# Optimization experiments

Measured on AMD Instinct MI355X. Metric: run time of the kernel, lower is better.

## Reference

```python
import jax, jax.numpy as jnp
import numpy as np

# 8 corner offsets of the trilinear cell: (8, 3)
_OFFS = jnp.array([[i, j, k] for i in (0, 1) for j in (0, 1) for k in (0, 1)], dtype=jnp.int32)


def _gridding(cloud, R):
    """Trilinear scatter of points into an RxRxR occupancy-weight grid.

    cloud: (b, n, 3) with coords in [-0.5, 0.5] (already divided by scale).
    Returns (b, R, R, R) grid where each point adds trilinear weights to its
    8 neighboring cells (the GRNet gridding_distance forward kernel).
    """
    b, n, _ = cloud.shape
    v = (cloud + 0.5) * R                      # continuous voxel coords in [0, R)
    lower = jnp.floor(v)
    frac = v - lower                           # (b, n, 3) in [0, 1)
    lower = lower.astype(jnp.int32)
    nb = lower[:, :, None, :] + _OFFS[None, None]              # (b, n, 8, 3)
    # per-axis trilinear weight: (1 - frac) for the low corner, frac for the high
    w_d = jnp.where(_OFFS[None, None] == 0,
                    1.0 - frac[:, :, None, :], frac[:, :, None, :])  # (b, n, 8, 3)
    w = jnp.prod(w_d, axis=-1)                                  # (b, n, 8)
    valid = jnp.all((nb >= 0) & (nb < R), axis=-1)              # (b, n, 8)
    w = jnp.where(valid, w, 0.0)
    nbc = jnp.clip(nb, 0, R - 1)
    flat = (nbc[..., 0] * R + nbc[..., 1]) * R + nbc[..., 2]    # (b, n, 8)
    batch_off = jnp.arange(b, dtype=jnp.int32)[:, None, None] * (R * R * R)
    idx = (flat + batch_off).reshape(-1)
    grid = jnp.zeros((b * R * R * R,), cloud.dtype).at[idx].add(w.reshape(-1))
    return grid.reshape(b, R, R, R)


def setup_inputs() -> dict:
    key = jax.random.key(0)
    k1, k2 = jax.random.split(key)
    R = 128
    B, N1, N2 = 16, 65536, 65536
    # coords in [-(R-2)/2, (R-2)/2] so that after /scale they are inside (-0.5, 0.5)
    pred = (jax.random.uniform(k1, (B, N1, 3), jnp.float32) - 0.5) * (R - 2)
    gt = (jax.random.uniform(k2, (B, N2, 3), jnp.float32) - 0.5) * (R - 2)
    return {"pred_cloud": pred, "gt_cloud": gt, "scale": R}


def reference(pred_cloud, gt_cloud, scale):
    pred = pred_cloud / scale
    gt = gt_cloud / scale
    return _gridding(pred, scale), _gridding(gt, scale)
```

## Files before the change

### kernel.cpp

```cpp
#include <hip/hip_runtime.h>
#include <stdint.h>


constexpr int R    = 128;
constexpr int R3c  = R * R * R;
constexpr int BPG  = 256;
constexpr int NBLK = 512;
constexpr int BLKT = 512;
constexpr int NCH  = 8;
constexpr int MAXBINS = 8192;

constexpr size_t WS_HIST = 0;
constexpr size_t WS_CS   = 16u << 20;
constexpr size_t WS_TOT  = 17u << 20;
constexpr size_t WS_BASE = 18u << 20;
constexpr size_t WS_QREC = 20u << 20;
constexpr size_t WS_REC  = 40u << 20;

typedef float f4v __attribute__((ext_vector_type(4)));

__device__ __forceinline__ uint32_t quant1(float p) {
    const float S = 16384.0f;
    const uint32_t QMAX = (126u << 14) | 16383u;
    float v = p + 64.0f;
    return min(__float2uint_rn(fmaxf(v, 0.0f) * S), QMAX);
}

__device__ __forceinline__ uint2 pack_rec(uint32_t xq, uint32_t yq, uint32_t zq) {
    return make_uint2(xq | (yq << 21), (yq >> 11) | (zq << 10));
}
__device__ __forceinline__ void unpack_rec(uint2 r, uint32_t& xq, uint32_t& yq, uint32_t& zq) {
    xq = r.x & 0x1FFFFFu;
    yq = (r.x >> 21) | ((r.y & 0x3FFu) << 11);
    zq = (r.y >> 10) & 0x1FFFFFu;
}

__device__ __forceinline__ void load_point(
    const float* __restrict__ pred, const float* __restrict__ gt,
    int i, int total1, int n1, int n2, int B,
    float& px, float& py, float& pz, int& cb)
{
    const float* p;
    if (i < total1) { p = pred + (size_t)i * 3; cb = i / n1; }
    else { int j = i - total1; p = gt + (size_t)j * 3; cb = B + j / n2; }
    px = p[0]; py = p[1]; pz = p[2];
}

__device__ __forceinline__ void region_range(uint32_t xq, uint32_t yq, uint32_t zq,
                                             int& rx0, int& rx1, int& ry0, int& ry1,
                                             int& rz0, int& rz1)
{
    int ix = xq >> 14, iy = yq >> 14, iz = zq >> 14;
    rx0 = ix >> 4; rx1 = (ix + 1) >> 4;
    ry0 = iy >> 4; ry1 = (iy + 1) >> 4;
    rz0 = iz >> 5; rz1 = (iz + 1) >> 5;
}

__global__ __launch_bounds__(BLKT, 2) void bin_hist_qrec(
    const float* __restrict__ pred, const float* __restrict__ gt,
    int total1, int P, int n1, int n2, int B, int ppb, int vec4ok,
    uint16_t* __restrict__ hist, uint2* __restrict__ qrec, int NBINS)
{
    __shared__ uint32_t h[MAXBINS];
    for (int j = threadIdx.x; j < NBINS; j += BLKT) h[j] = 0;
    __syncthreads();

    int s = blockIdx.x * ppb, e = min(s + ppb, P);
    if (vec4ok) {
        bool isgt = (s >= total1);
        const float* src = isgt ? gt + (size_t)(s - total1) * 3
                                : pred + (size_t)s * 3;
        const int n = isgt ? n2 : n1;
        const int cb0 = isgt ? B : 0;
        const int loff = isgt ? total1 : 0;
        const float4* src4 = (const float4*)src;
        int ngrp = (e - s) >> 2;
        for (int g = threadIdx.x; g < ngrp; g += BLKT) {
            float4 a = src4[g * 3 + 0];
            float4 b4 = src4[g * 3 + 1];
            float4 c4 = src4[g * 3 + 2];
            int li = (s + g * 4) - loff;
            int hbase = (cb0 + li / n) * BPG;
            float xs[4] = {a.x, a.w, b4.z, c4.y};
            float ys[4] = {a.y, b4.x, b4.w, c4.z};
            float zs[4] = {a.z, b4.y, c4.x, c4.w};
            uint2 rec[4];
            #pragma unroll
            for (int q = 0; q < 4; ++q) {
                uint32_t xq = quant1(xs[q]), yq = quant1(ys[q]), zq = quant1(zs[q]);
                rec[q] = pack_rec(xq, yq, zq);
                int rx0, rx1, ry0, ry1, rz0, rz1;
                region_range(xq, yq, zq, rx0, rx1, ry0, ry1, rz0, rz1);
                for (int aa = rx0; aa <= rx1; ++aa)
                    for (int bb = ry0; bb <= ry1; ++bb)
                        for (int cc = rz0; cc <= rz1; ++cc)
                            atomicAdd(&h[hbase + (aa << 5) + (bb << 2) + cc], 1u);
            }
            uint4* q4 = (uint4*)(qrec + (size_t)s + (size_t)g * 4);
            q4[0] = make_uint4(rec[0].x, rec[0].y, rec[1].x, rec[1].y);
            q4[1] = make_uint4(rec[2].x, rec[2].y, rec[3].x, rec[3].y);
        }
    } else {
        for (int i = s + threadIdx.x; i < e; i += BLKT) {
            float px, py, pz; int cb;
            load_point(pred, gt, i, total1, n1, n2, B, px, py, pz, cb);
            uint32_t xq = quant1(px), yq = quant1(py), zq = quant1(pz);
            qrec[i] = pack_rec(xq, yq, zq);
            int rx0, rx1, ry0, ry1, rz0, rz1;
            region_range(xq, yq, zq, rx0, rx1, ry0, ry1, rz0, rz1);
            int base = cb * BPG;
            for (int a = rx0; a <= rx1; ++a)
                for (int b = ry0; b <= ry1; ++b)
                    for (int c = rz0; c <= rz1; ++c)
                        atomicAdd(&h[base + (a << 5) + (b << 2) + c], 1u);
        }
    }
    __syncthreads();
    uint16_t* o = hist + (size_t)blockIdx.x * NBINS;
    for (int j = threadIdx.x; j < NBINS; j += BLKT) o[j] = (uint16_t)h[j];
}

__global__ __launch_bounds__(256) void scan_chunk(
    const uint16_t* __restrict__ hist, uint32_t* __restrict__ cs, int NBINS)
{
    int tid = blockIdx.x * 256 + threadIdx.x;
    if (tid >= NCH * NBINS) return;
    int c = tid / NBINS, j = tid - c * NBINS;
    int b0 = c * (NBLK / NCH);
    uint32_t s = 0;
    for (int b = b0; b < b0 + NBLK / NCH; ++b)
        s += hist[(size_t)b * NBINS + j];
    cs[c * NBINS + j] = s;
}

__global__ __launch_bounds__(256) void scan_fin(
    uint16_t* __restrict__ hist, const uint32_t* __restrict__ cs,
    uint32_t* __restrict__ tot, int NBINS)
{
    int tid = blockIdx.x * 256 + threadIdx.x;
    if (tid >= NCH * NBINS) return;
    int c = tid / NBINS, j = tid - c * NBINS;
    uint32_t run = 0;
    for (int cc = 0; cc < c; ++cc) run += cs[cc * NBINS + j];
    int b0 = c * (NBLK / NCH);
    for (int b = b0; b < b0 + NBLK / NCH; ++b) {
        size_t k = (size_t)b * NBINS + j;
        uint32_t t = hist[k];
        hist[k] = (uint16_t)run;
        run += t;
    }
    if (c == NCH - 1) tot[j] = run;
}

__global__ __launch_bounds__(256) void scan_base(
    const uint32_t* __restrict__ tot, uint32_t* __restrict__ base, int NBINS)
{
    __shared__ uint32_t part[256];
    int t = threadIdx.x;
    int chunk = NBINS / 256;
    uint32_t s = 0;
    for (int i = 0; i < chunk; ++i) s += tot[t * chunk + i];
    part[t] = s;
    __syncthreads();
    if (t == 0) {
        uint32_t run = 0;
        for (int i = 0; i < 256; ++i) { uint32_t v = part[i]; part[i] = run; run += v; }
    }
    __syncthreads();
    uint32_t run = part[t];
    for (int i = 0; i < chunk; ++i) {
        base[t * chunk + i] = run;
        run += tot[t * chunk + i];
    }
    if (t == 255) base[NBINS] = run;
}

__global__ __launch_bounds__(BLKT, 2) void bin_scatter_qrec(
    const uint2* __restrict__ qrec,
    int total1, int P, int n1, int n2, int B, int ppb, int vec4ok,
    const uint16_t* __restrict__ hist, const uint32_t* __restrict__ base,
    uint2* __restrict__ records, int NBINS)
{
    __shared__ uint32_t cur[MAXBINS];
    const uint16_t* hrow = hist + (size_t)blockIdx.x * NBINS;
    for (int j = threadIdx.x; j < NBINS; j += BLKT)
        cur[j] = base[j] + (uint32_t)hrow[j];
    __syncthreads();

    int s = blockIdx.x * ppb, e = min(s + ppb, P);
    if (vec4ok) {
        bool isgt = (s >= total1);
        const int n = isgt ? n2 : n1;
        const int cb0 = isgt ? B : 0;
        const int loff = isgt ? total1 : 0;
        const uint4* qr4 = (const uint4*)(qrec + (size_t)s);
        int ngrp = (e - s) >> 2;
        for (int g = threadIdx.x; g < ngrp; g += BLKT) {
            uint4 q0 = qr4[2 * g];
            uint4 q1 = qr4[2 * g + 1];
            uint2 rec[4] = {make_uint2(q0.x, q0.y), make_uint2(q0.z, q0.w),
                            make_uint2(q1.x, q1.y), make_uint2(q1.z, q1.w)};
            int li = (s + g * 4) - loff;
            int bb = (cb0 + li / n) * BPG;
            #pragma unroll
            for (int q = 0; q < 4; ++q) {
                uint32_t xq, yq, zq;
                unpack_rec(rec[q], xq, yq, zq);
                int rx0, rx1, ry0, ry1, rz0, rz1;
                region_range(xq, yq, zq, rx0, rx1, ry0, ry1, rz0, rz1);
                for (int aa = rx0; aa <= rx1; ++aa)
                    for (int b2 = ry0; b2 <= ry1; ++b2)
                        for (int cc = rz0; cc <= rz1; ++cc) {
                            uint32_t slot =
                                atomicAdd(&cur[bb + (aa << 5) + (b2 << 2) + cc], 1u);
                            records[slot] = rec[q];
                        }
            }
        }
    } else {
        for (int i = s + threadIdx.x; i < e; i += BLKT) {
            int cb;
            if (i < total1) cb = i / n1;
            else            cb = B + (i - total1) / n2;
            uint2 rec = qrec[i];
            uint32_t xq, yq, zq;
            unpack_rec(rec, xq, yq, zq);
            int rx0, rx1, ry0, ry1, rz0, rz1;
            region_range(xq, yq, zq, rx0, rx1, ry0, ry1, rz0, rz1);
            int bb = cb * BPG;
            for (int a = rx0; a <= rx1; ++a)
                for (int b = ry0; b <= ry1; ++b)
                    for (int c = rz0; c <= rz1; ++c) {
                        uint32_t slot = atomicAdd(&cur[bb + (a << 5) + (b << 2) + c], 1u);
                        records[slot] = rec;
                    }
        }
    }
}

__global__ __launch_bounds__(256) void accum_kernel(
    const uint32_t* __restrict__ base, const uint2* __restrict__ records,
    float* __restrict__ out)
{
    __shared__ float tile[16 * 16 * 32];
    int bin = blockIdx.x;
    int cb = bin >> 8;
    int region = bin & 255;
    int rx = region >> 5, ry = (region >> 2) & 7, rz = region & 3;

    float4* t4 = (float4*)tile;
    for (int t = threadIdx.x; t < 2048; t += 256)
        t4[t] = make_float4(0.f, 0.f, 0.f, 0.f);
    __syncthreads();

    uint32_t s = base[bin], e = base[bin + 1];
    const float FQ = 6.103515625e-05f;
    for (uint32_t r = s + threadIdx.x; r < e; r += 256) {
        uint32_t xq, yq, zq;
        unpack_rec(records[r], xq, yq, zq);
        int ix = xq >> 14, iy = yq >> 14, iz = zq >> 14;
        float fx = (float)(xq & 16383u) * FQ;
        float fy = (float)(yq & 16383u) * FQ;
        float fz = (float)(zq & 16383u) * FQ;
        float wx[2] = {1.0f - fx, fx};
        float wy[2] = {1.0f - fy, fy};
        float wz[2] = {1.0f - fz, fz};
        #pragma unroll
        for (int dx = 0; dx < 2; ++dx) {
            int cx = ix + dx;
            if ((cx >> 4) != rx) continue;
            #pragma unroll
            for (int dy = 0; dy < 2; ++dy) {
                int cy = iy + dy;
                if ((cy >> 4) != ry) continue;
                float wxy = wx[dx] * wy[dy];
                #pragma unroll
                for (int dz = 0; dz < 2; ++dz) {
                    int cz = iz + dz;
                    if ((cz >> 5) != rz) continue;
                    atomicAdd(&tile[(((cx & 15) << 4) + (cy & 15)) * 32 + (cz & 31)],
                              wxy * wz[dz]);
                }
            }
        }
    }
    __syncthreads();

    float* gout = out + (size_t)cb * R3c;
    for (int w = threadIdx.x; w < 2048; w += 256) {
        int lin = w * 4;
        int lx = lin >> 9, rem = lin & 511, ly = rem >> 5, lz = rem & 31;
        int X = rx * 16 + lx, Y = ry * 16 + ly, Z = rz * 32 + lz;
        f4v v = ((const f4v*)tile)[w];
        __builtin_nontemporal_store(v, (f4v*)&gout[((size_t)X * R + Y) * R + Z]);
    }
}

__device__ __forceinline__ void point_math_f(float px, float py, float pz,
                                             int& ix, int& iy, int& iz,
                                             float& fx, float& fy, float& fz)
{
    const float inv = 1.0f / 128.0f;
    float vx = (px * inv + 0.5f) * 128.0f;
    float vy = (py * inv + 0.5f) * 128.0f;
    float vz = (pz * inv + 0.5f) * 128.0f;
    float lx = floorf(vx), ly = floorf(vy), lz = floorf(vz);
    fx = vx - lx; fy = vy - ly; fz = vz - lz;
    ix = min(max((int)lx, 0), R - 2);
    iy = min(max((int)ly, 0), R - 2);
    iz = min(max((int)lz, 0), R - 2);
}

__global__ __launch_bounds__(256) void gridding_scatter(
    const float* __restrict__ cloud, float* __restrict__ grid,
    int total_pts, int n_per_batch)
{
    int idx = blockIdx.x * blockDim.x + threadIdx.x;
    if (idx >= total_pts) return;
    int b = idx / n_per_batch;
    const float* p = cloud + (size_t)idx * 3;
    int ix, iy, iz; float fx, fy, fz;
    point_math_f(p[0], p[1], p[2], ix, iy, iz, fx, fy, fz);
    float wx[2] = {1.0f - fx, fx};
    float wy[2] = {1.0f - fy, fy};
    float wz[2] = {1.0f - fz, fz};
    float* gb = grid + (size_t)b * R3c;
    #pragma unroll
    for (int dx = 0; dx < 2; ++dx)
        #pragma unroll
        for (int dy = 0; dy < 2; ++dy) {
            float wxy = wx[dx] * wy[dy];
            #pragma unroll
            for (int dz = 0; dz < 2; ++dz)
                atomicAdd(gb + ((size_t)(ix + dx) * R + (iy + dy)) * R + (iz + dz),
                          wxy * wz[dz]);
        }
}

extern "C" void kernel_launch(void* const* d_in, const int* in_sizes, int n_in,
                              void* d_out, int out_size, void* d_ws, size_t ws_size,
                              hipStream_t stream) {
    const float* pred = (const float*)d_in[0];
    const float* gt   = (const float*)d_in[1];
    float* out = (float*)d_out;

    int total1 = in_sizes[0] / 3;
    int total2 = in_sizes[1] / 3;
    int B  = out_size / (2 * R3c);
    int n1 = total1 / B;
    int n2 = total2 / B;
    int NBINS = 2 * B * BPG;
    int P  = total1 + total2;
    int ppb = (P + NBLK - 1) / NBLK;

    size_t ws_need = WS_REC + (size_t)8 * P * 8;
    if (ws_size < ws_need || NBINS > MAXBINS || NBINS % 256 != 0) {
        hipMemsetAsync(d_out, 0, (size_t)out_size * sizeof(float), stream);
        gridding_scatter<<<(total1 + 255) / 256, 256, 0, stream>>>(pred, out, total1, n1);
        gridding_scatter<<<(total2 + 255) / 256, 256, 0, stream>>>(
            gt, out + (size_t)B * R3c, total2, n2);
        return;
    }

    int vec4ok = (ppb % 4 == 0) && (total1 % ppb == 0) && (P % ppb == 0) &&
                 (n1 % 4 == 0) && (n2 % 4 == 0);

    uint16_t* hist  = (uint16_t*)((char*)d_ws + WS_HIST);
    uint32_t* cs    = (uint32_t*)((char*)d_ws + WS_CS);
    uint32_t* tot   = (uint32_t*)((char*)d_ws + WS_TOT);
    uint32_t* basep = (uint32_t*)((char*)d_ws + WS_BASE);
    uint2*    qrec  = (uint2*)((char*)d_ws + WS_QREC);
    uint2*    recs  = (uint2*)((char*)d_ws + WS_REC);

    int scan_thr = NCH * NBINS;

    bin_hist_qrec<<<NBLK, BLKT, 0, stream>>>(pred, gt, total1, P, n1, n2, B, ppb,
                                             vec4ok, hist, qrec, NBINS);
    scan_chunk<<<(scan_thr + 255) / 256, 256, 0, stream>>>(hist, cs, NBINS);
    scan_fin<<<(scan_thr + 255) / 256, 256, 0, stream>>>(hist, cs, tot, NBINS);
    scan_base<<<1, 256, 0, stream>>>(tot, basep, NBINS);
    bin_scatter_qrec<<<NBLK, BLKT, 0, stream>>>(qrec, total1, P, n1, n2, B, ppb,
                                                vec4ok, hist, basep, recs, NBINS);
    accum_kernel<<<NBINS, 256, 0, stream>>>(basep, recs, out);
}
```

Baseline: 392.6 us.

## Shrink per-block histograms to one cloud's bins and simplify prefix scan

```diff
diff --git a/kernel.cpp b/kernel.cpp
--- a/kernel.cpp
+++ b/kernel.cpp
@@ -7,15 +7,13 @@
 constexpr int BPG  = 256;
 constexpr int NBLK = 512;
 constexpr int BLKT = 512;
-constexpr int NCH  = 8;
-constexpr int MAXBINS = 8192;
+constexpr int MAXB = 128;
 
 constexpr size_t WS_HIST = 0;
-constexpr size_t WS_CS   = 16u << 20;
-constexpr size_t WS_TOT  = 17u << 20;
-constexpr size_t WS_BASE = 18u << 20;
-constexpr size_t WS_QREC = 20u << 20;
-constexpr size_t WS_REC  = 40u << 20;
+constexpr size_t WS_TOT  = 768u << 10;
+constexpr size_t WS_BASE = 1u << 20;
+constexpr size_t WS_QREC = 2u << 20;
+constexpr size_t WS_REC  = 20u << 20;
 
 typedef float f4v __attribute__((ext_vector_type(4)));
 
@@ -35,17 +33,6 @@
     zq = (r.y >> 10) & 0x1FFFFFu;
 }
 
-__device__ __forceinline__ void load_point(
-    const float* __restrict__ pred, const float* __restrict__ gt,
-    int i, int total1, int n1, int n2, int B,
-    float& px, float& py, float& pz, int& cb)
-{
-    const float* p;
-    if (i < total1) { p = pred + (size_t)i * 3; cb = i / n1; }
-    else { int j = i - total1; p = gt + (size_t)j * 3; cb = B + j / n2; }
-    px = p[0]; py = p[1]; pz = p[2];
-}
-
 __device__ __forceinline__ void region_range(uint32_t xq, uint32_t yq, uint32_t zq,
                                              int& rx0, int& rx1, int& ry0, int& ry1,
                                              int& rz0, int& rz1)
@@ -56,31 +43,27 @@
     rz0 = iz >> 5; rz1 = (iz + 1) >> 5;
 }
 
-__global__ __launch_bounds__(BLKT, 2) void bin_hist_qrec(
+__global__ __launch_bounds__(BLKT) void bin_hist_qrec(
     const float* __restrict__ pred, const float* __restrict__ gt,
-    int total1, int P, int n1, int n2, int B, int ppb, int vec4ok,
-    uint16_t* __restrict__ hist, uint2* __restrict__ qrec, int NBINS)
-{
-    __shared__ uint32_t h[MAXBINS];
-    for (int j = threadIdx.x; j < NBINS; j += BLKT) h[j] = 0;
-    __syncthreads();
-
-    int s = blockIdx.x * ppb, e = min(s + ppb, P);
-    if (vec4ok) {
+    int total1, int P, int ppb,
+    uint32_t* __restrict__ hist, uint2* __restrict__ qrec)
+{
+    __shared__ uint32_t h[BPG];
+    if (threadIdx.x < BPG) h[threadIdx.x] = 0;
+    __syncthreads();
+
+    int s = blockIdx.x * ppb;
+    if (s < P) {
+        int e = min(s + ppb, P);
         bool isgt = (s >= total1);
         const float* src = isgt ? gt + (size_t)(s - total1) * 3
                                 : pred + (size_t)s * 3;
-        const int n = isgt ? n2 : n1;
-        const int cb0 = isgt ? B : 0;
-        const int loff = isgt ? total1 : 0;
         const float4* src4 = (const float4*)src;
         int ngrp = (e - s) >> 2;
         for (int g = threadIdx.x; g < ngrp; g += BLKT) {
-            float4 a = src4[g * 3 + 0];
+            float4 a  = src4[g * 3 + 0];
             float4 b4 = src4[g * 3 + 1];
             float4 c4 = src4[g * 3 + 2];
-            int li = (s + g * 4) - loff;
-            int hbase = (cb0 + li / n) * BPG;
             float xs[4] = {a.x, a.w, b4.z, c4.y};
             float ys[4] = {a.y, b4.x, b4.w, c4.z};
             float zs[4] = {a.z, b4.y, c4.x, c4.w};
@@ -94,62 +77,35 @@
                 for (int aa = rx0; aa <= rx1; ++aa)
                     for (int bb = ry0; bb <= ry1; ++bb)
                         for (int cc = rz0; cc <= rz1; ++cc)
-                            atomicAdd(&h[hbase + (aa << 5) + (bb << 2) + cc], 1u);
+                            atomicAdd(&h[(aa << 5) + (bb << 2) + cc], 1u);
             }
             uint4* q4 = (uint4*)(qrec + (size_t)s + (size_t)g * 4);
             q4[0] = make_uint4(rec[0].x, rec[0].y, rec[1].x, rec[1].y);
             q4[1] = make_uint4(rec[2].x, rec[2].y, rec[3].x, rec[3].y);
         }
-    } else {
-        for (int i = s + threadIdx.x; i < e; i += BLKT) {
-            float px, py, pz; int cb;
-            load_point(pred, gt, i, total1, n1, n2, B, px, py, pz, cb);
-            uint32_t xq = quant1(px), yq = quant1(py), zq = quant1(pz);
-            qrec[i] = pack_rec(xq, yq, zq);
-            int rx0, rx1, ry0, ry1, rz0, rz1;
-            region_range(xq, yq, zq, rx0, rx1, ry0, ry1, rz0, rz1);
-            int base = cb * BPG;
-            for (int a = rx0; a <= rx1; ++a)
-                for (int b = ry0; b <= ry1; ++b)
-                    for (int c = rz0; c <= rz1; ++c)
-                        atomicAdd(&h[base + (a << 5) + (b << 2) + c], 1u);
-        }
-    }
-    __syncthreads();
-    uint16_t* o = hist + (size_t)blockIdx.x * NBINS;
-    for (int j = threadIdx.x; j < NBINS; j += BLKT) o[j] = (uint16_t)h[j];
-}
-
-__global__ __launch_bounds__(256) void scan_chunk(
-    const uint16_t* __restrict__ hist, uint32_t* __restrict__ cs, int NBINS)
-{
-    int tid = blockIdx.x * 256 + threadIdx.x;
-    if (tid >= NCH * NBINS) return;
-    int c = tid / NBINS, j = tid - c * NBINS;
-    int b0 = c * (NBLK / NCH);
-    uint32_t s = 0;
-    for (int b = b0; b < b0 + NBLK / NCH; ++b)
-        s += hist[(size_t)b * NBINS + j];
-    cs[c * NBINS + j] = s;
-}
-
-__global__ __launch_bounds__(256) void scan_fin(
-    uint16_t* __restrict__ hist, const uint32_t* __restrict__ cs,
-    uint32_t* __restrict__ tot, int NBINS)
-{
-    int tid = blockIdx.x * 256 + threadIdx.x;
-    if (tid >= NCH * NBINS) return;
-    int c = tid / NBINS, j = tid - c * NBINS;
+    }
+    __syncthreads();
+    if (threadIdx.x < BPG)
+        hist[(size_t)blockIdx.x * BPG + threadIdx.x] = h[threadIdx.x];
+}
+
+__global__ __launch_bounds__(256) void scan1(
+    uint32_t* __restrict__ hist, uint32_t* __restrict__ tot,
+    int B, int nb1, int bpg1, int bpg2, int NBINS)
+{
+    int j = blockIdx.x * 256 + threadIdx.x;
+    if (j >= NBINS) return;
+    int cb = j >> 8, l = j & 255;
+    int first = (cb < B) ? cb * bpg1 : nb1 + (cb - B) * bpg2;
+    int cnt   = (cb < B) ? bpg1 : bpg2;
     uint32_t run = 0;
-    for (int cc = 0; cc < c; ++cc) run += cs[cc * NBINS + j];
-    int b0 = c * (NBLK / NCH);
-    for (int b = b0; b < b0 + NBLK / NCH; ++b) {
-        size_t k = (size_t)b * NBINS + j;
-        uint32_t t = hist[k];
-        hist[k] = (uint16_t)run;
+    for (int k = 0; k < cnt; ++k) {
+        size_t idx = (size_t)(first + k) * BPG + l;
+        uint32_t t = hist[idx];
+        hist[idx] = run;
         run += t;
     }
-    if (c == NCH - 1) tot[j] = run;
+    tot[j] = run;
 }
 
 __global__ __launch_bounds__(256) void scan_base(
@@ -175,64 +131,42 @@
     if (t == 255) base[NBINS] = run;
 }
 
-__global__ __launch_bounds__(BLKT, 2) void bin_scatter_qrec(
+__global__ __launch_bounds__(BLKT) void bin_scatter_qrec(
     const uint2* __restrict__ qrec,
-    int total1, int P, int n1, int n2, int B, int ppb, int vec4ok,
-    const uint16_t* __restrict__ hist, const uint32_t* __restrict__ base,
-    uint2* __restrict__ records, int NBINS)
-{
-    __shared__ uint32_t cur[MAXBINS];
-    const uint16_t* hrow = hist + (size_t)blockIdx.x * NBINS;
-    for (int j = threadIdx.x; j < NBINS; j += BLKT)
-        cur[j] = base[j] + (uint32_t)hrow[j];
-    __syncthreads();
-
-    int s = blockIdx.x * ppb, e = min(s + ppb, P);
-    if (vec4ok) {
-        bool isgt = (s >= total1);
-        const int n = isgt ? n2 : n1;
-        const int cb0 = isgt ? B : 0;
-        const int loff = isgt ? total1 : 0;
-        const uint4* qr4 = (const uint4*)(qrec + (size_t)s);
-        int ngrp = (e - s) >> 2;
-        for (int g = threadIdx.x; g < ngrp; g += BLKT) {
-            uint4 q0 = qr4[2 * g];
-            uint4 q1 = qr4[2 * g + 1];
-            uint2 rec[4] = {make_uint2(q0.x, q0.y), make_uint2(q0.z, q0.w),
-                            make_uint2(q1.x, q1.y), make_uint2(q1.z, q1.w)};
-            int li = (s + g * 4) - loff;
-            int bb = (cb0 + li / n) * BPG;
-            #pragma unroll
-            for (int q = 0; q < 4; ++q) {
-                uint32_t xq, yq, zq;
-                unpack_rec(rec[q], xq, yq, zq);
-                int rx0, rx1, ry0, ry1, rz0, rz1;
-                region_range(xq, yq, zq, rx0, rx1, ry0, ry1, rz0, rz1);
-                for (int aa = rx0; aa <= rx1; ++aa)
-                    for (int b2 = ry0; b2 <= ry1; ++b2)
-                        for (int cc = rz0; cc <= rz1; ++cc) {
-                            uint32_t slot =
-                                atomicAdd(&cur[bb + (aa << 5) + (b2 << 2) + cc], 1u);
-                            records[slot] = rec[q];
-                        }
-            }
-        }
-    } else {
-        for (int i = s + threadIdx.x; i < e; i += BLKT) {
-            int cb;
-            if (i < total1) cb = i / n1;
-            else            cb = B + (i - total1) / n2;
-            uint2 rec = qrec[i];
+    int total1, int P, int n1, int n2, int B, int ppb,
+    const uint32_t* __restrict__ hist, const uint32_t* __restrict__ base,
+    uint2* __restrict__ records)
+{
+    int s = blockIdx.x * ppb;
+    if (s >= P) return;
+    int cb = (s < total1) ? (s / n1) : (B + (s - total1) / n2);
+
+    __shared__ uint32_t cur[BPG];
+    if (threadIdx.x < BPG)
+        cur[threadIdx.x] = base[cb * BPG + threadIdx.x] +
+                           hist[(size_t)blockIdx.x * BPG + threadIdx.x];
+    __syncthreads();
+
+    int e = min(s + ppb, P);
+    const uint4* qr4 = (const uint4*)(qrec + (size_t)s);
+    int ngrp = (e - s) >> 2;
+    for (int g = threadIdx.x; g < ngrp; g += BLKT) {
+        uint4 q0 = qr4[2 * g];
+        uint4 q1 = qr4[2 * g + 1];
+        uint2 rec[4] = {make_uint2(q0.x, q0.y), make_uint2(q0.z, q0.w),
+                        make_uint2(q1.x, q1.y), make_uint2(q1.z, q1.w)};
+        #pragma unroll
+        for (int q = 0; q < 4; ++q) {
             uint32_t xq, yq, zq;
-            unpack_rec(rec, xq, yq, zq);
+            unpack_rec(rec[q], xq, yq, zq);
             int rx0, rx1, ry0, ry1, rz0, rz1;
             region_range(xq, yq, zq, rx0, rx1, ry0, ry1, rz0, rz1);
-            int bb = cb * BPG;
-            for (int a = rx0; a <= rx1; ++a)
-                for (int b = ry0; b <= ry1; ++b)
-                    for (int c = rz0; c <= rz1; ++c) {
-                        uint32_t slot = atomicAdd(&cur[bb + (a << 5) + (b << 2) + c], 1u);
-                        records[slot] = rec;
+            for (int aa = rx0; aa <= rx1; ++aa)
+                for (int b2 = ry0; b2 <= ry1; ++b2)
+                    for (int cc = rz0; cc <= rz1; ++cc) {
+                        uint32_t slot =
+                            atomicAdd(&cur[(aa << 5) + (b2 << 2) + cc], 1u);
+                        records[slot] = rec[q];
                     }
         }
     }
@@ -353,8 +287,12 @@
     int P  = total1 + total2;
     int ppb = (P + NBLK - 1) / NBLK;
 
+    bool fastok = (ppb % 4 == 0) && (n1 % ppb == 0) && (n2 % ppb == 0) &&
+                  (n1 > 0) && (n2 > 0) && (B > 0) && (B <= MAXB) &&
+                  (NBINS % 256 == 0) &&
+                  (total1 % n1 == 0) && (total2 % n2 == 0);
     size_t ws_need = WS_REC + (size_t)8 * P * 8;
-    if (ws_size < ws_need || NBINS > MAXBINS || NBINS % 256 != 0) {
+    if (!fastok || ws_size < ws_need) {
         hipMemsetAsync(d_out, 0, (size_t)out_size * sizeof(float), stream);
         gridding_scatter<<<(total1 + 255) / 256, 256, 0, stream>>>(pred, out, total1, n1);
         gridding_scatter<<<(total2 + 255) / 256, 256, 0, stream>>>(
@@ -362,24 +300,20 @@
         return;
     }
 
-    int vec4ok = (ppb % 4 == 0) && (total1 % ppb == 0) && (P % ppb == 0) &&
-                 (n1 % 4 == 0) && (n2 % 4 == 0);
-
-    uint16_t* hist  = (uint16_t*)((char*)d_ws + WS_HIST);
-    uint32_t* cs    = (uint32_t*)((char*)d_ws + WS_CS);
+    uint32_t* hist  = (uint32_t*)((char*)d_ws + WS_HIST);
     uint32_t* tot   = (uint32_t*)((char*)d_ws + WS_TOT);
     uint32_t* basep = (uint32_t*)((char*)d_ws + WS_BASE);
     uint2*    qrec  = (uint2*)((char*)d_ws + WS_QREC);
     uint2*    recs  = (uint2*)((char*)d_ws + WS_REC);
 
-    int scan_thr = NCH * NBINS;
-
-    bin_hist_qrec<<<NBLK, BLKT, 0, stream>>>(pred, gt, total1, P, n1, n2, B, ppb,
-                                             vec4ok, hist, qrec, NBINS);
-    scan_chunk<<<(scan_thr + 255) / 256, 256, 0, stream>>>(hist, cs, NBINS);
-    scan_fin<<<(scan_thr + 255) / 256, 256, 0, stream>>>(hist, cs, tot, NBINS);
+    int nb1  = total1 / ppb;
+    int bpg1 = n1 / ppb;
+    int bpg2 = n2 / ppb;
+
+    bin_hist_qrec<<<NBLK, BLKT, 0, stream>>>(pred, gt, total1, P, ppb, hist, qrec);
+    scan1<<<(NBINS + 255) / 256, 256, 0, stream>>>(hist, tot, B, nb1, bpg1, bpg2, NBINS);
     scan_base<<<1, 256, 0, stream>>>(tot, basep, NBINS);
     bin_scatter_qrec<<<NBLK, BLKT, 0, stream>>>(qrec, total1, P, n1, n2, B, ppb,
-                                                vec4ok, hist, basep, recs, NBINS);
+                                                hist, basep, recs);
     accum_kernel<<<NBINS, 256, 0, stream>>>(basep, recs, out);
 }
```

Result: no change. 386.2 us (-1.6%).
